# Performance work log

Hardware: AMD Instinct MI355X
Metric: run time of the kernel (lower is better)

The kernel has to match this reference:

```python
import jax, jax.numpy as jnp
import numpy as np

B, T, N, F, H, E = 8, 16, 10000, 64, 64, 1000000
M = B * N  # flattened node count per timestep
NUM_CLASSES = 3


def setup_inputs() -> dict:
    key = jax.random.key(0)
    ks = jax.random.split(key, 10)
    s = 1.0 / np.sqrt(H)
    return {
        "graph_seq": jax.random.normal(ks[0], (B, T, N, F), dtype=jnp.float32),
        "edge_index_seq": jax.random.randint(ks[1], (T, 2, E), 0, M, dtype=jnp.int32),
        "W_gcn": jax.random.normal(ks[2], (F, H), dtype=jnp.float32) / np.sqrt(F),
        "b_gcn": jnp.zeros((H,), dtype=jnp.float32),
        "W_ih": jax.random.uniform(ks[3], (4 * H, H), jnp.float32, -s, s),
        "W_hh": jax.random.uniform(ks[4], (4 * H, H), jnp.float32, -s, s),
        "b_ih": jax.random.uniform(ks[5], (4 * H,), jnp.float32, -s, s),
        "b_hh": jax.random.uniform(ks[6], (4 * H,), jnp.float32, -s, s),
        "W_fc": jax.random.uniform(ks[7], (NUM_CLASSES, H), jnp.float32, -s, s),
        "b_fc": jax.random.uniform(ks[8], (NUM_CLASSES,), jnp.float32, -s, s),
    }


def _forward(graph_seq, edge_index_seq, W_gcn, b_gcn, W_ih, W_hh, b_ih, b_hh, W_fc, b_fc):
    # GCNConv: x' = D^{-1/2}(A+I)D^{-1/2} (x W) + b, applied on flattened (B*N) nodes per timestep.
    xw = jnp.einsum('btnf,fh->btnh', graph_seq, W_gcn)        # [B,T,N,H]
    xw_t = xw.transpose(1, 0, 2, 3).reshape(T, M, H)          # [T, B*N, H], node index = b*N + n

    def gcn_step(_, inp):
        x, ei = inp                                           # x: [M,H], ei: [2,E]
        src, dst = ei[0], ei[1]
        deg = jax.ops.segment_sum(jnp.ones((E,), x.dtype), dst, num_segments=M) + 1.0  # +1 self loop
        dinv = jax.lax.rsqrt(deg)
        coef = dinv[src] * dinv[dst]                          # [E]
        agg = jax.ops.segment_sum(x[src] * coef[:, None], dst, num_segments=M)
        out = agg + x * (dinv * dinv)[:, None] + b_gcn        # self-loop term + bias
        pooled = out.reshape(B, N, H).mean(axis=1)            # mean over nodes -> [B,H]
        return None, pooled

    _, pooled_seq = jax.lax.scan(gcn_step, None, (xw_t, edge_index_seq))  # [T,B,H]

    def lstm_step(carry, x_t):
        h, c = carry
        z = x_t @ W_ih.T + h @ W_hh.T + b_ih + b_hh           # [B,4H], gate order i,f,g,o
        i, f, g, o = jnp.split(z, 4, axis=-1)
        c = jax.nn.sigmoid(f) * c + jax.nn.sigmoid(i) * jnp.tanh(g)
        h = jax.nn.sigmoid(o) * jnp.tanh(c)
        return (h, c), None

    h0 = jnp.zeros((B, H), dtype=graph_seq.dtype)
    (h_last, _), _ = jax.lax.scan(lstm_step, (h0, h0), pooled_seq)
    return h_last @ W_fc.T + b_fc                             # [B,3]


def reference(graph_seq, edge_index_seq, W_gcn, b_gcn, W_ih, W_hh, b_ih, b_hh, W_fc, b_fc):
    return _forward(graph_seq, edge_index_seq, W_gcn, b_gcn, W_ih, W_hh, b_ih, b_hh, W_fc, b_fc)
```

## Files before the change

### kernel.cpp

```cpp
#include <hip/hip_runtime.h>
#include <hip/hip_bf16.h>

#define BB 8
#define TT 16
#define NNODE 10000
#define FF 64
#define HH 64
#define EE 1000000
#define MM 80000
#define NCLS 3

#define NCHUNK 32
#define NPC 2500
#define CAPB 36032
#define NSEG_H 16
#define HW 20000
#define NSEG_B 32
#define EPW 7816
#define WCAP 144
#define FLUSH_THR 96
#define GPAD 16

__global__ __launch_bounds__(256) void k_hist(const int* __restrict__ ei,
                                              unsigned int* __restrict__ part, int t0) {
    __shared__ unsigned int h[HW];
    int seg = blockIdx.x, tloc = blockIdx.y, tg = t0 + tloc;
    for (int i = threadIdx.x; i < HW; i += 256) h[i] = 0u;
    __syncthreads();
    const uint4* dstp = (const uint4*)(ei + (size_t)tg * 2 * EE + EE
                                       + (size_t)seg * (EE / NSEG_H));
    for (int i = threadIdx.x; i < (EE / NSEG_H) / 4; i += 256) {
        uint4 d4 = dstp[i];
        atomicAdd(&h[d4.x >> 2], 1u << ((d4.x & 3u) * 8u));
        atomicAdd(&h[d4.y >> 2], 1u << ((d4.y & 3u) * 8u));
        atomicAdd(&h[d4.z >> 2], 1u << ((d4.z & 3u) * 8u));
        atomicAdd(&h[d4.w >> 2], 1u << ((d4.w & 3u) * 8u));
    }
    __syncthreads();
    unsigned int* outp = part + ((size_t)tloc * NSEG_H + seg) * HW;
    for (int i = threadIdx.x; i < HW; i += 256) outp[i] = h[i];
}

__global__ __launch_bounds__(256) void k_mdeg(const unsigned int* __restrict__ part,
                                              float* __restrict__ dinv) {
    int w = blockIdx.x * 256 + threadIdx.x;
    int tloc = blockIdx.y;
    if (w >= HW) return;
    const unsigned int* p = part + (size_t)tloc * NSEG_H * HW;
    unsigned int s = 0;
#pragma unroll
    for (int k = 0; k < NSEG_H; k++) s += p[(size_t)k * HW + w];
    float4 r;
    r.x = rsqrtf((float)(s & 255u) + 1.0f);
    r.y = rsqrtf((float)((s >> 8) & 255u) + 1.0f);
    r.z = rsqrtf((float)((s >> 16) & 255u) + 1.0f);
    r.w = rsqrtf((float)((s >> 24) & 255u) + 1.0f);
    *(float4*)(dinv + (size_t)tloc * MM + (size_t)w * 4) = r;
}

__global__ __launch_bounds__(256) void k_part(const int* __restrict__ ei,
                                              unsigned int* __restrict__ buck,
                                              unsigned int* __restrict__ gcur, int t0) {
    __shared__ unsigned int stg[4][NCHUNK][WCAP];
    __shared__ unsigned int cur[4][NCHUNK];
    int wave = threadIdx.x >> 6, lane = threadIdx.x & 63;
    int tloc = blockIdx.y, tg = t0 + tloc;
    if (lane < NCHUNK) cur[wave][lane] = 0u;

    int wseg = blockIdx.x * 4 + wave;
    int e0 = wseg * EPW;
    int e1 = e0 + EPW; if (e1 > EE) e1 = EE;
    const uint4* src4 = (const uint4*)(ei + (size_t)tg * 2 * EE);
    const uint4* dst4 = (const uint4*)(ei + (size_t)tg * 2 * EE + EE);
    unsigned int* gc = gcur + (size_t)tloc * NCHUNK * GPAD;
    unsigned int* bk = buck + (size_t)tloc * NCHUNK * CAPB;

    int i40 = e0 >> 2, i41 = e1 >> 2;
    int nIter = (i41 - i40 + 63) >> 6;
    for (int k = 0; k < nIter; k++) {
        int i4 = i40 + k * 64 + lane;
        if (i4 < i41) {
            uint4 s4 = src4[i4];
            uint4 d4 = dst4[i4];
            unsigned int ss[4] = {s4.x, s4.y, s4.z, s4.w};
            unsigned int dd[4] = {d4.x, d4.y, d4.z, d4.w};
#pragma unroll
            for (int j = 0; j < 4; j++) {
                unsigned int ck = (unsigned int)(((unsigned long long)ss[j] * 1717987ull) >> 32);
                unsigned int so = ss[j] - ck * NPC;
                unsigned int p = atomicAdd(&cur[wave][ck], 1u);
                if (p < WCAP) stg[wave][ck][p] = (so << 17) | dd[j];
            }
        }
        unsigned int cnt = (lane < NCHUNK) ? cur[wave][lane] : 0u;
        unsigned long long mask = __ballot(cnt >= FLUSH_THR);
        while (mask) {
            int ck = __ffsll((unsigned long long)mask) - 1;
            mask &= mask - 1;
            unsigned int n = cur[wave][ck];
            if (n > WCAP) n = WCAP;
            unsigned int gp = 0;
            if (lane == 0) gp = atomicAdd(&gc[ck * GPAD], n);
            gp = (unsigned int)__shfl((int)gp, 0);
            if (gp + n <= CAPB) {
                for (unsigned int j = lane; j < n; j += 64)
                    bk[(size_t)ck * CAPB + gp + j] = stg[wave][ck][j];
            }
            if (lane == 0) cur[wave][ck] = 0u;
        }
    }
    for (int ck = 0; ck < NCHUNK; ck++) {
        unsigned int n = cur[wave][ck];
        if (n > WCAP) n = WCAP;
        if (n > 0u) {
            unsigned int gp = 0;
            if (lane == 0) gp = atomicAdd(&gc[ck * GPAD], n);
            gp = (unsigned int)__shfl((int)gp, 0);
            if (gp + n <= CAPB) {
                for (unsigned int j = lane; j < n; j += 64)
                    bk[(size_t)ck * CAPB + gp + j] = stg[wave][ck][j];
            }
        }
    }
}

__global__ __launch_bounds__(256) void k_scat(const float* __restrict__ g,
                                              const float* __restrict__ dinv,
                                              const unsigned int* __restrict__ buck,
                                              const unsigned int* __restrict__ gcur,
                                              float* __restrict__ yp, int t0) {
    __shared__ float a[NPC * BB];
    int c = blockIdx.x, tloc = blockIdx.y, tg = t0 + tloc;
    for (int i = threadIdx.x; i < NPC * BB; i += 256) a[i] = 0.0f;
    __syncthreads();

    const float* dv = dinv + (size_t)tloc * MM;
    unsigned int n = gcur[((size_t)tloc * NCHUNK + c) * GPAD];
    if (n > CAPB) n = CAPB;
    const unsigned int* bk = buck + ((size_t)tloc * NCHUNK + c) * CAPB;

    unsigned int n4 = n >> 2;
    for (unsigned int i = threadIdx.x; i < n4; i += 256) {
        uint4 r = ((const uint4*)bk)[i];
        unsigned int rec[4] = {r.x, r.y, r.z, r.w};
#pragma unroll
        for (int k = 0; k < 4; k++) {
            unsigned int d = rec[k] & 0x1FFFFu;
            unsigned int so = rec[k] >> 17;
            unsigned int b = (unsigned int)(((unsigned long long)d * 429497ull) >> 32);
            atomicAdd(&a[so * BB + b], dv[d]);
        }
    }
    {
        unsigned int i = (n4 << 2) + threadIdx.x;
        if (i < n) {
            unsigned int rec = bk[i];
            unsigned int d = rec & 0x1FFFFu;
            unsigned int so = rec >> 17;
            unsigned int b = (unsigned int)(((unsigned long long)d * 429497ull) >> 32);
            atomicAdd(&a[so * BB + b], dv[d]);
        }
    }
    __syncthreads();

    int lane = threadIdx.x & 63;
    int wave = threadIdx.x >> 6;
    int sub = lane >> 4;
    int f0 = (lane & 15) << 2;
    int b_c = c >> 2;
    const size_t base_g = ((size_t)(b_c * TT + tg) * NNODE + (size_t)(c & 3) * NPC) * FF;
    const float* dvc = dv + (size_t)c * NPC;

    float acc[BB][4];
#pragma unroll
    for (int b = 0; b < BB; b++)
#pragma unroll
        for (int q = 0; q < 4; q++) acc[b][q] = 0.0f;

    for (int gi = wave; gi < NPC / 4; gi += 4) {
        int joff = gi * 4 + sub;
        float dvj = dvc[joff];
        const float4 g4 = *(const float4*)(g + base_g + (size_t)joff * FF + f0);
        const float4 a0 = *(const float4*)(&a[joff * BB]);
        const float4 a1 = *(const float4*)(&a[joff * BB + 4]);
        float av[BB] = {a0.x, a0.y, a0.z, a0.w, a1.x, a1.y, a1.z, a1.w};
        float wv[BB];
#pragma unroll
        for (int b = 0; b < BB; b++)
            wv[b] = dvj * (av[b] + (b == b_c ? dvj : 0.0f));
#pragma unroll
        for (int b = 0; b < BB; b++) {
            acc[b][0] = fmaf(g4.x, wv[b], acc[b][0]);
            acc[b][1] = fmaf(g4.y, wv[b], acc[b][1]);
            acc[b][2] = fmaf(g4.z, wv[b], acc[b][2]);
            acc[b][3] = fmaf(g4.w, wv[b], acc[b][3]);
        }
    }

    __syncthreads();
#pragma unroll
    for (int b = 0; b < BB; b++)
#pragma unroll
        for (int q = 0; q < 4; q++) {
            float v = acc[b][q];
            v += __shfl_xor(v, 16);
            v += __shfl_xor(v, 32);
            acc[b][q] = v;
        }
    if (sub == 0) {
#pragma unroll
        for (int b = 0; b < BB; b++)
#pragma unroll
            for (int q = 0; q < 4; q++)
                a[wave * (BB * FF) + b * FF + f0 + q] = acc[b][q];
    }
    __syncthreads();
    for (int idx = threadIdx.x; idx < BB * FF; idx += 256) {
        float s = a[idx] + a[BB * FF + idx] + a[2 * BB * FF + idx] + a[3 * BB * FF + idx];
        yp[((size_t)tg * NCHUNK + c) * (BB * FF) + idx] = s;
    }
}

__global__ __launch_bounds__(256) void k_lstm(const float* __restrict__ yp,
                                              const float* __restrict__ Wg,
                                              const float* __restrict__ bg,
                                              const float* __restrict__ Wih,
                                              const float* __restrict__ Whh,
                                              const float* __restrict__ bih,
                                              const float* __restrict__ bhh,
                                              const float* __restrict__ Wfc,
                                              const float* __restrict__ bfc,
                                              float* __restrict__ out) {
    int b = blockIdx.x;
    int r = threadIdx.x;

    __shared__ float ys[TT][FF];
    __shared__ float xs[TT][HH];
    __shared__ float hs[HH], cs[HH], zs[4 * HH];

    for (int idx = r; idx < TT * FF; idx += 256) {
        int t = idx >> 6, f = idx & 63;
        const float* p = yp + ((size_t)t * NCHUNK * BB + b) * FF + f;
        float s = 0.0f;
#pragma unroll
        for (int c = 0; c < NCHUNK; c++) s += p[(size_t)c * BB * FF];
        ys[t][f] = s;
    }
    __syncthreads();

    for (int idx = r; idx < TT * HH; idx += 256) {
        int t = idx >> 6, h = idx & 63;
        float s = 0.0f;
#pragma unroll
        for (int f = 0; f < FF; f++) s = fmaf(ys[t][f], Wg[f * HH + h], s);
        xs[t][h] = s * (1.0f / NNODE) + bg[h];
    }

    float wih[HH], whh[HH];
#pragma unroll
    for (int k = 0; k < HH; k++) {
        wih[k] = Wih[r * HH + k];
        whh[k] = Whh[r * HH + k];
    }
    float bias = bih[r] + bhh[r];

    if (r < HH) { hs[r] = 0.0f; cs[r] = 0.0f; }
    __syncthreads();

    for (int t = 0; t < TT; t++) {
        float acc = bias;
#pragma unroll
        for (int k = 0; k < HH; k++)
            acc = fmaf(wih[k], xs[t][k], fmaf(whh[k], hs[k], acc));
        zs[r] = acc;
        __syncthreads();
        if (r < HH) {
            float iv = zs[r], fv = zs[HH + r], gv = zs[2 * HH + r], ov = zs[3 * HH + r];
            float si = 1.0f / (1.0f + expf(-iv));
            float sf = 1.0f / (1.0f + expf(-fv));
            float so = 1.0f / (1.0f + expf(-ov));
            float cc = sf * cs[r] + si * tanhf(gv);
            cs[r] = cc;
            hs[r] = so * tanhf(cc);
        }
        __syncthreads();
    }

    if (r < NCLS) {
        float s = bfc[r];
#pragma unroll
        for (int k = 0; k < HH; k++) s = fmaf(hs[k], Wfc[r * HH + k], s);
        out[b * NCLS + r] = s;
    }
}

extern "C" void kernel_launch(void* const* d_in, const int* in_sizes, int n_in,
                              void* d_out, int out_size, void* d_ws, size_t ws_size,
                              hipStream_t stream) {
    const float* g   = (const float*)d_in[0];
    const int*   ei  = (const int*)d_in[1];
    const float* Wg  = (const float*)d_in[2];
    const float* bg  = (const float*)d_in[3];
    const float* Wih = (const float*)d_in[4];
    const float* Whh = (const float*)d_in[5];
    const float* bih = (const float*)d_in[6];
    const float* bhh = (const float*)d_in[7];
    const float* Wfc = (const float*)d_in[8];
    const float* bfc = (const float*)d_in[9];
    float* out = (float*)d_out;

    char* ws = (char*)d_ws;
    float* yp = (float*)ws;
    const size_t ypBytes = (size_t)TT * NCHUNK * BB * FF * sizeof(float);

    const size_t sz_dinv = (size_t)MM * 4;
    const size_t sz_part = (size_t)NSEG_H * HW * 4;
    const size_t sz_buck = (size_t)NCHUNK * CAPB * 4;
    const size_t sz_gcur = (size_t)NCHUNK * GPAD * 4;
    const size_t per_t = sz_dinv + sz_part + sz_buck + sz_gcur;

    size_t avail = (ws_size > ypBytes) ? ws_size - ypBytes : 0;
    int Tg = (int)(avail / per_t);
    if (Tg > TT) Tg = TT;
    if (Tg < 1) Tg = 1;

    float* dinv        = (float*)(ws + ypBytes);
    unsigned int* part = (unsigned int*)(ws + ypBytes + (size_t)Tg * sz_dinv);
    unsigned int* buck = (unsigned int*)(ws + ypBytes + (size_t)Tg * (sz_dinv + sz_part));
    unsigned int* gcur = (unsigned int*)(ws + ypBytes + (size_t)Tg * (sz_dinv + sz_part + sz_buck));

    for (int t0 = 0; t0 < TT; t0 += Tg) {
        int tc = (TT - t0 < Tg) ? (TT - t0) : Tg;
        hipMemsetAsync(gcur, 0, (size_t)tc * NCHUNK * GPAD * 4, stream);

        dim3 gh(NSEG_H, tc);
        k_hist<<<gh, 256, 0, stream>>>(ei, part, t0);

        dim3 gm((HW + 255) / 256, tc);
        k_mdeg<<<gm, 256, 0, stream>>>(part, dinv);

        dim3 gp(NSEG_B, tc);
        k_part<<<gp, 256, 0, stream>>>(ei, buck, gcur, t0);

        dim3 gs(NCHUNK, tc);
        k_scat<<<gs, 256, 0, stream>>>(g, dinv, buck, gcur, yp, t0);
    }

    k_lstm<<<BB, 256, 0, stream>>>(yp, Wg, bg, Wih, Whh, bih, bhh, Wfc, bfc, out);
}
```

Before: 372.2 us.

## Use per-wave private edge buckets with finer chunks and packed degree bytes

Switches the edge partition from 32 chunks with globally atomic-appended buckets to 80 chunks of 1000 nodes. Each wave now owns a private fixed-capacity region per chunk, which removes the global atomics and the gcur memset. Degrees are stored as packed bytes and turned into rsqrt factors on the fly inside the scatter. The scatter kernel moves to 512 threads, folds the dinv scaling into the shared accumulator before the g-weighted reduction, and adds a separate fold kernel ahead of the LSTM. In exchange it relies on fixed per-wave capacities (RCAP 176, WCAP 48), so records past those limits are silently dropped.

```diff
diff --git a/kernel.cpp b/kernel.cpp
--- a/kernel.cpp
+++ b/kernel.cpp
@@ -10,16 +10,17 @@
 #define MM 80000
 #define NCLS 3
 
-#define NCHUNK 32
-#define NPC 2500
-#define CAPB 36032
+#define NCHUNK 80
+#define NPC 1000
 #define NSEG_H 16
 #define HW 20000
 #define NSEG_B 32
+#define NW 128
 #define EPW 7816
-#define WCAP 144
-#define FLUSH_THR 96
-#define GPAD 16
+#define WCAP 48
+#define FLUSH_THR 24
+#define RCAP 176
+#define RSZ 177
 
 __global__ __launch_bounds__(256) void k_hist(const int* __restrict__ ei,
                                               unsigned int* __restrict__ part, int t0) {
@@ -42,7 +43,7 @@
 }
 
 __global__ __launch_bounds__(256) void k_mdeg(const unsigned int* __restrict__ part,
-                                              float* __restrict__ dinv) {
+                                              unsigned int* __restrict__ degb) {
     int w = blockIdx.x * 256 + threadIdx.x;
     int tloc = blockIdx.y;
     if (w >= HW) return;
@@ -50,30 +51,25 @@
     unsigned int s = 0;
 #pragma unroll
     for (int k = 0; k < NSEG_H; k++) s += p[(size_t)k * HW + w];
-    float4 r;
-    r.x = rsqrtf((float)(s & 255u) + 1.0f);
-    r.y = rsqrtf((float)((s >> 8) & 255u) + 1.0f);
-    r.z = rsqrtf((float)((s >> 16) & 255u) + 1.0f);
-    r.w = rsqrtf((float)((s >> 24) & 255u) + 1.0f);
-    *(float4*)(dinv + (size_t)tloc * MM + (size_t)w * 4) = r;
+    degb[(size_t)tloc * HW + w] = s;
 }
 
 __global__ __launch_bounds__(256) void k_part(const int* __restrict__ ei,
-                                              unsigned int* __restrict__ buck,
-                                              unsigned int* __restrict__ gcur, int t0) {
+                                              unsigned int* __restrict__ buck, int t0) {
     __shared__ unsigned int stg[4][NCHUNK][WCAP];
     __shared__ unsigned int cur[4][NCHUNK];
+    __shared__ unsigned int gct[4][NCHUNK];
     int wave = threadIdx.x >> 6, lane = threadIdx.x & 63;
     int tloc = blockIdx.y, tg = t0 + tloc;
-    if (lane < NCHUNK) cur[wave][lane] = 0u;
+    if (lane < 64) { cur[wave][lane] = 0u; gct[wave][lane] = 0u; }
+    if (lane < NCHUNK - 64) { cur[wave][64 + lane] = 0u; gct[wave][64 + lane] = 0u; }
 
     int wseg = blockIdx.x * 4 + wave;
     int e0 = wseg * EPW;
     int e1 = e0 + EPW; if (e1 > EE) e1 = EE;
     const uint4* src4 = (const uint4*)(ei + (size_t)tg * 2 * EE);
     const uint4* dst4 = (const uint4*)(ei + (size_t)tg * 2 * EE + EE);
-    unsigned int* gc = gcur + (size_t)tloc * NCHUNK * GPAD;
-    unsigned int* bk = buck + (size_t)tloc * NCHUNK * CAPB;
+    unsigned int* bkt = buck + ((size_t)tloc * NCHUNK * NW + wseg) * RSZ;
 
     int i40 = e0 >> 2, i41 = e1 >> 2;
     int nIter = (i41 - i40 + 63) >> 6;
@@ -86,142 +82,146 @@
             unsigned int dd[4] = {d4.x, d4.y, d4.z, d4.w};
 #pragma unroll
             for (int j = 0; j < 4; j++) {
-                unsigned int ck = (unsigned int)(((unsigned long long)ss[j] * 1717987ull) >> 32);
+                unsigned int ck = (unsigned int)(((unsigned long long)ss[j] * 4294968ull) >> 32);
                 unsigned int so = ss[j] - ck * NPC;
                 unsigned int p = atomicAdd(&cur[wave][ck], 1u);
                 if (p < WCAP) stg[wave][ck][p] = (so << 17) | dd[j];
             }
         }
-        unsigned int cnt = (lane < NCHUNK) ? cur[wave][lane] : 0u;
-        unsigned long long mask = __ballot(cnt >= FLUSH_THR);
-        while (mask) {
-            int ck = __ffsll((unsigned long long)mask) - 1;
-            mask &= mask - 1;
-            unsigned int n = cur[wave][ck];
-            if (n > WCAP) n = WCAP;
-            unsigned int gp = 0;
-            if (lane == 0) gp = atomicAdd(&gc[ck * GPAD], n);
-            gp = (unsigned int)__shfl((int)gp, 0);
-            if (gp + n <= CAPB) {
-                for (unsigned int j = lane; j < n; j += 64)
-                    bk[(size_t)ck * CAPB + gp + j] = stg[wave][ck][j];
+#pragma unroll
+        for (int half = 0; half < 2; half++) {
+            int nh = half ? (NCHUNK - 64) : 64;
+            unsigned int cnt = (lane < nh) ? cur[wave][half * 64 + lane] : 0u;
+            unsigned long long mask = __ballot(cnt >= FLUSH_THR);
+            while (mask) {
+                int ck = half * 64 + (__ffsll((unsigned long long)mask) - 1);
+                mask &= mask - 1;
+                unsigned int n = cur[wave][ck];
+                if (n > WCAP) n = WCAP;
+                unsigned int gp = gct[wave][ck];
+                unsigned int nw = (gp + n <= RCAP) ? n : ((gp < RCAP) ? (RCAP - gp) : 0u);
+                unsigned int* rg = bkt + (size_t)ck * NW * RSZ;
+                if (lane < nw) rg[1 + gp + lane] = stg[wave][ck][lane];
+                if (lane == 0) { gct[wave][ck] = gp + nw; cur[wave][ck] = 0u; }
             }
-            if (lane == 0) cur[wave][ck] = 0u;
         }
     }
     for (int ck = 0; ck < NCHUNK; ck++) {
         unsigned int n = cur[wave][ck];
         if (n > WCAP) n = WCAP;
         if (n > 0u) {
-            unsigned int gp = 0;
-            if (lane == 0) gp = atomicAdd(&gc[ck * GPAD], n);
-            gp = (unsigned int)__shfl((int)gp, 0);
-            if (gp + n <= CAPB) {
-                for (unsigned int j = lane; j < n; j += 64)
-                    bk[(size_t)ck * CAPB + gp + j] = stg[wave][ck][j];
-            }
-        }
-    }
-}
-
-__global__ __launch_bounds__(256) void k_scat(const float* __restrict__ g,
-                                              const float* __restrict__ dinv,
-                                              const unsigned int* __restrict__ buck,
-                                              const unsigned int* __restrict__ gcur,
-                                              float* __restrict__ yp, int t0) {
+            unsigned int gp = gct[wave][ck];
+            unsigned int nw = (gp + n <= RCAP) ? n : ((gp < RCAP) ? (RCAP - gp) : 0u);
+            unsigned int* rg = bkt + (size_t)ck * NW * RSZ;
+            if (lane < nw) rg[1 + gp + lane] = stg[wave][ck][lane];
+            if (lane == 0) gct[wave][ck] = gp + nw;
+        }
+    }
+    for (int ck = lane; ck < NCHUNK; ck += 64)
+        bkt[(size_t)ck * NW * RSZ] = gct[wave][ck];
+}
+
+__global__ __launch_bounds__(512, 8) void k_scat(const float* __restrict__ g,
+                                                 const unsigned int* __restrict__ degb,
+                                                 const unsigned int* __restrict__ buck,
+                                                 float* __restrict__ yp, int t0) {
     __shared__ float a[NPC * BB];
     int c = blockIdx.x, tloc = blockIdx.y, tg = t0 + tloc;
-    for (int i = threadIdx.x; i < NPC * BB; i += 256) a[i] = 0.0f;
-    __syncthreads();
-
-    const float* dv = dinv + (size_t)tloc * MM;
-    unsigned int n = gcur[((size_t)tloc * NCHUNK + c) * GPAD];
-    if (n > CAPB) n = CAPB;
-    const unsigned int* bk = buck + ((size_t)tloc * NCHUNK + c) * CAPB;
-
-    unsigned int n4 = n >> 2;
-    for (unsigned int i = threadIdx.x; i < n4; i += 256) {
-        uint4 r = ((const uint4*)bk)[i];
-        unsigned int rec[4] = {r.x, r.y, r.z, r.w};
-#pragma unroll
-        for (int k = 0; k < 4; k++) {
-            unsigned int d = rec[k] & 0x1FFFFu;
-            unsigned int so = rec[k] >> 17;
-            unsigned int b = (unsigned int)(((unsigned long long)d * 429497ull) >> 32);
-            atomicAdd(&a[so * BB + b], dv[d]);
-        }
-    }
-    {
-        unsigned int i = (n4 << 2) + threadIdx.x;
-        if (i < n) {
-            unsigned int rec = bk[i];
+    int wave = threadIdx.x >> 6, lane = threadIdx.x & 63;
+
+    for (int i = threadIdx.x; i < NPC * BB; i += 512) a[i] = 0.0f;
+    __syncthreads();
+
+    const unsigned char* degc = (const unsigned char*)(degb + (size_t)tloc * HW);
+    const unsigned int* bkc = buck + ((size_t)tloc * NCHUNK + c) * NW * RSZ;
+
+    for (int r = wave; r < NW; r += 8) {
+        const unsigned int* rg = bkc + (size_t)r * RSZ;
+        unsigned int cnt = rg[0];
+        if (cnt > RCAP) cnt = RCAP;
+        for (unsigned int i = lane; i < cnt; i += 64) {
+            unsigned int rec = rg[1 + i];
             unsigned int d = rec & 0x1FFFFu;
             unsigned int so = rec >> 17;
             unsigned int b = (unsigned int)(((unsigned long long)d * 429497ull) >> 32);
-            atomicAdd(&a[so * BB + b], dv[d]);
-        }
-    }
-    __syncthreads();
-
-    int lane = threadIdx.x & 63;
-    int wave = threadIdx.x >> 6;
-    int sub = lane >> 4;
-    int f0 = (lane & 15) << 2;
-    int b_c = c >> 2;
-    const size_t base_g = ((size_t)(b_c * TT + tg) * NNODE + (size_t)(c & 3) * NPC) * FF;
-    const float* dvc = dv + (size_t)c * NPC;
-
-    float acc[BB][4];
+            atomicAdd(&a[so * BB + b], rsqrtf((float)degc[d] + 1.0f));
+        }
+    }
+    __syncthreads();
+
+    int b_c = c / 10, coff = c - b_c * 10;
+    int jbase = c * NPC;
+    for (int j = threadIdx.x; j < NPC; j += 512) {
+        float dvj = rsqrtf((float)degc[jbase + j] + 1.0f);
+        float* aj = &a[j * BB];
+#pragma unroll
+        for (int b = 0; b < BB; b++) {
+            float v = aj[b] + (b == b_c ? dvj : 0.0f);
+            aj[b] = dvj * v;
+        }
+    }
+    __syncthreads();
+
+    const float* gp = g + ((size_t)(b_c * TT + tg) * NNODE + (size_t)coff * NPC) * FF + lane;
+    float acc[BB];
+#pragma unroll
+    for (int b = 0; b < BB; b++) acc[b] = 0.0f;
+
+    for (int j0 = wave; j0 < NPC; j0 += 16) {
+        int j1 = j0 + 8;
+        bool h1 = (j1 < NPC);
+        float g0 = gp[(size_t)j0 * FF];
+        float g1 = h1 ? gp[(size_t)j1 * FF] : 0.0f;
+        const float4 a00 = *(const float4*)(&a[j0 * BB]);
+        const float4 a01 = *(const float4*)(&a[j0 * BB + 4]);
+        acc[0] = fmaf(g0, a00.x, acc[0]);
+        acc[1] = fmaf(g0, a00.y, acc[1]);
+        acc[2] = fmaf(g0, a00.z, acc[2]);
+        acc[3] = fmaf(g0, a00.w, acc[3]);
+        acc[4] = fmaf(g0, a01.x, acc[4]);
+        acc[5] = fmaf(g0, a01.y, acc[5]);
+        acc[6] = fmaf(g0, a01.z, acc[6]);
+        acc[7] = fmaf(g0, a01.w, acc[7]);
+        if (h1) {
+            const float4 a10 = *(const float4*)(&a[j1 * BB]);
+            const float4 a11 = *(const float4*)(&a[j1 * BB + 4]);
+            acc[0] = fmaf(g1, a10.x, acc[0]);
+            acc[1] = fmaf(g1, a10.y, acc[1]);
+            acc[2] = fmaf(g1, a10.z, acc[2]);
+            acc[3] = fmaf(g1, a10.w, acc[3]);
+            acc[4] = fmaf(g1, a11.x, acc[4]);
+            acc[5] = fmaf(g1, a11.y, acc[5]);
+            acc[6] = fmaf(g1, a11.z, acc[6]);
+            acc[7] = fmaf(g1, a11.w, acc[7]);
+        }
+    }
+
+    __syncthreads();
 #pragma unroll
     for (int b = 0; b < BB; b++)
-#pragma unroll
-        for (int q = 0; q < 4; q++) acc[b][q] = 0.0f;
-
-    for (int gi = wave; gi < NPC / 4; gi += 4) {
-        int joff = gi * 4 + sub;
-        float dvj = dvc[joff];
-        const float4 g4 = *(const float4*)(g + base_g + (size_t)joff * FF + f0);
-        const float4 a0 = *(const float4*)(&a[joff * BB]);
-        const float4 a1 = *(const float4*)(&a[joff * BB + 4]);
-        float av[BB] = {a0.x, a0.y, a0.z, a0.w, a1.x, a1.y, a1.z, a1.w};
-        float wv[BB];
-#pragma unroll
-        for (int b = 0; b < BB; b++)
-            wv[b] = dvj * (av[b] + (b == b_c ? dvj : 0.0f));
-#pragma unroll
-        for (int b = 0; b < BB; b++) {
-            acc[b][0] = fmaf(g4.x, wv[b], acc[b][0]);
-            acc[b][1] = fmaf(g4.y, wv[b], acc[b][1]);
-            acc[b][2] = fmaf(g4.z, wv[b], acc[b][2]);
-            acc[b][3] = fmaf(g4.w, wv[b], acc[b][3]);
-        }
-    }
-
-    __syncthreads();
-#pragma unroll
-    for (int b = 0; b < BB; b++)
-#pragma unroll
-        for (int q = 0; q < 4; q++) {
-            float v = acc[b][q];
-            v += __shfl_xor(v, 16);
-            v += __shfl_xor(v, 32);
-            acc[b][q] = v;
-        }
-    if (sub == 0) {
-#pragma unroll
-        for (int b = 0; b < BB; b++)
-#pragma unroll
-            for (int q = 0; q < 4; q++)
-                a[wave * (BB * FF) + b * FF + f0 + q] = acc[b][q];
-    }
-    __syncthreads();
-    for (int idx = threadIdx.x; idx < BB * FF; idx += 256) {
-        float s = a[idx] + a[BB * FF + idx] + a[2 * BB * FF + idx] + a[3 * BB * FF + idx];
+        a[wave * (BB * FF) + b * FF + lane] = acc[b];
+    __syncthreads();
+    {
+        int idx = threadIdx.x;
+        float s = 0.0f;
+#pragma unroll
+        for (int w = 0; w < 8; w++) s += a[w * (BB * FF) + idx];
         yp[((size_t)tg * NCHUNK + c) * (BB * FF) + idx] = s;
     }
 }
 
-__global__ __launch_bounds__(256) void k_lstm(const float* __restrict__ yp,
+__global__ __launch_bounds__(512) void k_fold(const float* __restrict__ yp,
+                                              float* __restrict__ y2) {
+    int t = blockIdx.x;
+    int idx = threadIdx.x;
+    const float* p = yp + (size_t)t * NCHUNK * BB * FF + idx;
+    float s = 0.0f;
+#pragma unroll 8
+    for (int u = 0; u < NCHUNK; u++) s += p[(size_t)u * BB * FF];
+    y2[(size_t)t * BB * FF + idx] = s;
+}
+
+__global__ __launch_bounds__(256) void k_lstm(const float* __restrict__ y2,
                                               const float* __restrict__ Wg,
                                               const float* __restrict__ bg,
                                               const float* __restrict__ Wih,
@@ -234,25 +234,15 @@
     int b = blockIdx.x;
     int r = threadIdx.x;
 
-    __shared__ float ys[TT][FF];
     __shared__ float xs[TT][HH];
     __shared__ float hs[HH], cs[HH], zs[4 * HH];
 
-    for (int idx = r; idx < TT * FF; idx += 256) {
-        int t = idx >> 6, f = idx & 63;
-        const float* p = yp + ((size_t)t * NCHUNK * BB + b) * FF + f;
-        float s = 0.0f;
-#pragma unroll
-        for (int c = 0; c < NCHUNK; c++) s += p[(size_t)c * BB * FF];
-        ys[t][f] = s;
-    }
-    __syncthreads();
-
     for (int idx = r; idx < TT * HH; idx += 256) {
         int t = idx >> 6, h = idx & 63;
+        const float* yt = y2 + ((size_t)t * BB + b) * FF;
         float s = 0.0f;
 #pragma unroll
-        for (int f = 0; f < FF; f++) s = fmaf(ys[t][f], Wg[f * HH + h], s);
+        for (int f = 0; f < FF; f++) s = fmaf(yt[f], Wg[f * HH + h], s);
         xs[t][h] = s * (1.0f / NNODE) + bg[h];
     }
 
@@ -312,39 +302,41 @@
     char* ws = (char*)d_ws;
     float* yp = (float*)ws;
     const size_t ypBytes = (size_t)TT * NCHUNK * BB * FF * sizeof(float);
-
-    const size_t sz_dinv = (size_t)MM * 4;
+    float* y2 = (float*)(ws + ypBytes);
+    const size_t y2Bytes = (size_t)TT * BB * FF * sizeof(float);
+    const size_t headBytes = ypBytes + y2Bytes;
+
     const size_t sz_part = (size_t)NSEG_H * HW * 4;
-    const size_t sz_buck = (size_t)NCHUNK * CAPB * 4;
-    const size_t sz_gcur = (size_t)NCHUNK * GPAD * 4;
-    const size_t per_t = sz_dinv + sz_part + sz_buck + sz_gcur;
-
-    size_t avail = (ws_size > ypBytes) ? ws_size - ypBytes : 0;
+    const size_t sz_degb = (size_t)HW * 4;
+    const size_t sz_buck = (size_t)NCHUNK * NW * RSZ * 4;
+    const size_t per_t = sz_part + sz_degb + sz_buck;
+
+    size_t avail = (ws_size > headBytes) ? ws_size - headBytes : 0;
     int Tg = (int)(avail / per_t);
     if (Tg > TT) Tg = TT;
     if (Tg < 1) Tg = 1;
 
-    float* dinv        = (float*)(ws + ypBytes);
-    unsigned int* part = (unsigned int*)(ws + ypBytes + (size_t)Tg * sz_dinv);
-    unsigned int* buck = (unsigned int*)(ws + ypBytes + (size_t)Tg * (sz_dinv + sz_part));
-    unsigned int* gcur = (unsigned int*)(ws + ypBytes + (size_t)Tg * (sz_dinv + sz_part + sz_buck));
+    size_t ofs = headBytes;
+    unsigned int* part = (unsigned int*)(ws + ofs); ofs += (size_t)Tg * sz_part;
+    unsigned int* degb = (unsigned int*)(ws + ofs); ofs += (size_t)Tg * sz_degb;
+    unsigned int* buck = (unsigned int*)(ws + ofs);
 
     for (int t0 = 0; t0 < TT; t0 += Tg) {
         int tc = (TT - t0 < Tg) ? (TT - t0) : Tg;
-        hipMemsetAsync(gcur, 0, (size_t)tc * NCHUNK * GPAD * 4, stream);
 
         dim3 gh(NSEG_H, tc);
         k_hist<<<gh, 256, 0, stream>>>(ei, part, t0);
 
         dim3 gm((HW + 255) / 256, tc);
-        k_mdeg<<<gm, 256, 0, stream>>>(part, dinv);
+        k_mdeg<<<gm, 256, 0, stream>>>(part, degb);
 
         dim3 gp(NSEG_B, tc);
-        k_part<<<gp, 256, 0, stream>>>(ei, buck, gcur, t0);
+        k_part<<<gp, 256, 0, stream>>>(ei, buck, t0);
 
         dim3 gs(NCHUNK, tc);
-        k_scat<<<gs, 256, 0, stream>>>(g, dinv, buck, gcur, yp, t0);
-    }
-
-    k_lstm<<<BB, 256, 0, stream>>>(yp, Wg, bg, Wih, Whh, bih, bhh, Wfc, bfc, out);
-}
+        k_scat<<<gs, 512, 0, stream>>>(g, degb, buck, yp, t0);
+    }
+
+    k_fold<<<TT, 512, 0, stream>>>(yp, y2);
+    k_lstm<<<BB, 256, 0, stream>>>(y2, Wg, bg, Wih, Whh, bih, bhh, Wfc, bfc, out);
+}
```

Measured after the change: 360.9 us. -3.0%, faster.
